# Kernel optimization log

Hardware: AMD Instinct MI355X
Metric: run time of the kernel (lower is better)

Reference implementation:

```python
import jax, jax.numpy as jnp
import numpy as np

D_BRICK = 512  # args.brick_vector_dimension
H = 512        # hidden width


def setup_inputs() -> dict:
    key = jax.random.key(0)
    ks = jax.random.split(key, 20)
    B, N = 4, 192

    def w(k, shape, fan_in):
        return jax.random.uniform(k, shape, jnp.float32, -1.0, 1.0) / np.sqrt(fan_in)

    return {
        "brick_vectors": jax.random.normal(ks[0], (B, N, D_BRICK), jnp.float32),
        "xy": jax.random.uniform(ks[1], (B, N, 2), jnp.float32),
        # linear_xy: 2 -> 512
        "W_xy": w(ks[2], (H, 2), 2), "b_xy": w(ks[3], (H,), 2),
        # linear_a: D -> 512
        "W_a": w(ks[4], (H, D_BRICK), D_BRICK), "b_a": w(ks[5], (H,), D_BRICK),
        # linear_b: 512 -> 512
        "W_b": w(ks[6], (H, H), H), "b_b": w(ks[7], (H,), H),
        # combination_a: 1024 -> 512
        "W_ca": w(ks[8], (H, 2 * H), 2 * H), "b_ca": w(ks[9], (H,), 2 * H),
        # combination_b: 512 -> 512
        "W_cb": w(ks[10], (H, H), H), "b_cb": w(ks[11], (H,), H),
        # combination_c: 512 -> 512
        "W_cc": w(ks[12], (H, H), H), "b_cc": w(ks[13], (H,), H),
        # edge_out: 512 -> 2
        "W_out": w(ks[14], (2, H), H), "b_out": w(ks[15], (2,), H),
    }


def reference(brick_vectors, xy, W_xy, b_xy, W_a, b_a, W_b, b_b,
              W_ca, b_ca, W_cb, b_cb, W_cc, b_cc, W_out, b_out):
    # per-brick feature MLP: (B, N, 512)
    f = jnp.einsum('bnd,hd->bnh', brick_vectors, W_a) + b_a \
        + jnp.einsum('bnt,ht->bnh', xy, W_xy) + b_xy
    f = jax.nn.relu(f)
    f = jax.nn.relu(jnp.einsum('bnh,gh->bng', f, W_b) + b_b)

    # combination_a on concat(f[b,j], f[b,i]) without materializing the
    # (B, N, N, 1024) tensor: split the weight into the two 512 halves.
    # edge[b,i,j] = cat(features_a, features_b) where features_a = f[b,j]
    # (expanded over dim 1) and features_b = f[b,i] (expanded over dim 2).
    W1, W2 = W_ca[:, :H], W_ca[:, H:]
    u = jnp.einsum('bnh,gh->bng', f, W1)  # contribution from f[b, j]
    v = jnp.einsum('bnh,gh->bng', f, W2)  # contribution from f[b, i]
    e = jax.nn.relu(u[:, None, :, :] + v[:, :, None, :] + b_ca)  # (B,N,N,512)

    e = jax.nn.relu(jnp.einsum('bijh,gh->bijg', e, W_cb) + b_cb)
    e = jax.nn.relu(jnp.einsum('bijh,gh->bijg', e, W_cc) + b_cc)
    return jnp.einsum('bijh,oh->bijo', e, W_out) + b_out  # (B, N, N, 2)
```

## Files before the change

### kernel.cpp

```cpp
#include <hip/hip_runtime.h>


typedef short  short8  __attribute__((ext_vector_type(8)));
typedef short  short4v __attribute__((ext_vector_type(4)));
typedef float  f32x4   __attribute__((ext_vector_type(4)));

#define LDSW 520

__device__ inline unsigned short f2bf(float x) {
  unsigned u = __float_as_uint(x);
  unsigned r = (u + 0x7FFFu + ((u >> 16) & 1u)) >> 16;
  return (unsigned short)r;
}

__device__ __host__ inline int wtile_off(int c, int k) {
  return ((c >> 4) * 16 + (k >> 5)) * 512 + (c & 15) * 32 + (k & 31);
}

template <int MT, int NT>
__device__ inline void zero_acc(f32x4 (&acc)[MT][NT]) {
#pragma unroll
  for (int mt = 0; mt < MT; ++mt)
#pragma unroll
    for (int nt = 0; nt < NT; ++nt) {
      f32x4 z = {0.f, 0.f, 0.f, 0.f};
      acc[mt][nt] = z;
    }
}

template <int MT, int NT>
__device__ inline void gemm_kloop(const short* E, const short* __restrict__ W,
                                  int lane, int nbase, f32x4 (&acc)[MT][NT]) {
  const int mrow = lane & 15, kg = lane >> 4;
  const short* El = E + mrow * LDSW + kg * 8;
  const short* Wl = W + (nbase >> 4) * 8192 + mrow * 32 + kg * 8;
  short8 wF[2][NT];
#pragma unroll
  for (int nt = 0; nt < NT; ++nt) wF[0][nt] = *(const short8*)(Wl + nt * 8192);
#pragma unroll
  for (int ks = 0; ks < 16; ++ks) {
    const int cur = ks & 1, nxt = cur ^ 1;
    if (ks < 15) {
      const int k1 = (ks + 1) * 512;
#pragma unroll
      for (int nt = 0; nt < NT; ++nt)
        wF[nxt][nt] = *(const short8*)(Wl + nt * 8192 + k1);
    }
    const int k0 = ks * 32;
    short8 e0 = *(const short8*)(El + k0);
#pragma unroll
    for (int mt = 0; mt < MT; ++mt) {
      const short8 ecur = e0;
      if (mt < MT - 1) e0 = *(const short8*)(El + (mt + 1) * 16 * LDSW + k0);
#pragma unroll
      for (int nt = 0; nt < NT; ++nt)
        acc[mt][nt] = __builtin_amdgcn_mfma_f32_16x16x32_bf16(
            wF[cur][nt], ecur, acc[mt][nt], 0, 0, 0);
    }
  }
}

template <int MT, int NT>
__device__ inline void store_relu_lds(short* E, const float* __restrict__ bias,
                                      int lane, int nbase, f32x4 (&acc)[MT][NT]) {
  const int mrow = lane & 15, kg = lane >> 4;
#pragma unroll
  for (int nt = 0; nt < NT; ++nt) {
    const int oc = nbase + nt * 16 + kg * 4;
    const float4 bs = *(const float4*)(bias + oc);
#pragma unroll
    for (int mt = 0; mt < MT; ++mt) {
      short4v s;
      s.x = (short)f2bf(fmaxf(acc[mt][nt][0] + bs.x, 0.f));
      s.y = (short)f2bf(fmaxf(acc[mt][nt][1] + bs.y, 0.f));
      s.z = (short)f2bf(fmaxf(acc[mt][nt][2] + bs.z, 0.f));
      s.w = (short)f2bf(fmaxf(acc[mt][nt][3] + bs.w, 0.f));
      *(short4v*)&E[(mt * 16 + mrow) * LDSW + oc] = s;
    }
  }
}

__global__ void prep_kernel(const float* __restrict__ Wa, const float* __restrict__ Wb,
                            const float* __restrict__ Wca, const float* __restrict__ Wcb,
                            const float* __restrict__ Wcc, const float* __restrict__ Wout,
                            short* __restrict__ outS) {
  const int tid = blockIdx.x * blockDim.x + threadIdx.x;
  const int stride = gridDim.x * blockDim.x;
  const int M = 262144;
  for (int i = tid; i < 6 * M + 1024; i += stride) {
    float x;
    int dst;
    if (i < M) {
      const int c = i >> 9, k = i & 511;
      x = Wa[i];
      dst = wtile_off(c, k);
    } else if (i < 2 * M) {
      const int t = i - M, c = t >> 9, k = t & 511;
      x = Wb[t];
      dst = M + wtile_off(c, k);
    } else if (i < 3 * M) {
      const int t = i - 2 * M, c = t >> 9, k = t & 511;
      x = Wca[c * 1024 + k];
      dst = 2 * M + wtile_off(c, k);
    } else if (i < 4 * M) {
      const int t = i - 3 * M, c = t >> 9, k = t & 511;
      x = Wca[c * 1024 + 512 + k];
      dst = 2 * M + wtile_off(512 + c, k);
    } else if (i < 5 * M) {
      const int t = i - 4 * M, c = t >> 9, k = t & 511;
      x = Wcb[t];
      dst = 4 * M + wtile_off(c, k);
    } else if (i < 6 * M) {
      const int t = i - 5 * M, c = t >> 9, k = t & 511;
      x = Wcc[t];
      dst = 5 * M + wtile_off(c, k);
    } else {
      x = Wout[i - 6 * M];
      dst = i;
    }
    outS[dst] = (short)f2bf(x);
  }
}

template <int MODE>
__global__ __launch_bounds__(256, 4) void node_layer(
    const void* __restrict__ Xin, const short* __restrict__ W,
    const float* __restrict__ bias, const float* __restrict__ xy,
    const float* __restrict__ Wxy, const float* __restrict__ bxy,
    void* __restrict__ Yout, float* __restrict__ vout, int colTiles) {
  __shared__ short X[64 * LDSW];
  __shared__ float xyl[128];
  const int tid = threadIdx.x, lane = tid & 63, wave = tid >> 6;
  const int rt = blockIdx.x / colTiles, ct = blockIdx.x % colTiles;
  const int row0 = rt * 64, c0 = ct * 64;

  if (MODE == 1) {
    const float* bv = (const float*)Xin;
    const int hc = (tid & 127) * 4, m0 = tid >> 7;
    for (int m = m0; m < 64; m += 2) {
      const float4 t = *(const float4*)(bv + (row0 + m) * 512 + hc);
      short4v s;
      s.x = (short)f2bf(t.x); s.y = (short)f2bf(t.y);
      s.z = (short)f2bf(t.z); s.w = (short)f2bf(t.w);
      *(short4v*)&X[m * LDSW + hc] = s;
    }
    if (tid < 128) xyl[tid] = xy[row0 * 2 + tid];
  } else {
    const short* xb = (const short*)Xin;
    const int hc = (tid & 63) * 8, m0 = tid >> 6;
    for (int m = m0; m < 64; m += 4)
      *(short8*)&X[m * LDSW + hc] = *(const short8*)(xb + (row0 + m) * 512 + hc);
  }
  __syncthreads();

  const int nbase = c0 + wave * 16;
  f32x4 acc[4][1];
  zero_acc<4, 1>(acc);
  gemm_kloop<4, 1>(X, W, lane, nbase, acc);

  const int mrow = lane & 15, kg = lane >> 4;
  const int oc = nbase + kg * 4;
  if (MODE == 3) {
    float* u = (float*)Yout;
#pragma unroll
    for (int mt = 0; mt < 4; ++mt) {
      const int row = row0 + mt * 16 + mrow;
      if (oc < 512) *(f32x4*)&u[row * 512 + oc] = acc[mt][0];
      else          *(f32x4*)&vout[row * 512 + oc - 512] = acc[mt][0];
    }
  } else {
    short* Y = (short*)Yout;
    const float4 bs = *(const float4*)(bias + oc);
    float b2[4] = {0.f, 0.f, 0.f, 0.f}, w0[4], w1[4];
    if (MODE == 1) {
      const float4 t = *(const float4*)(bxy + oc);
      b2[0] = t.x; b2[1] = t.y; b2[2] = t.z; b2[3] = t.w;
#pragma unroll
      for (int r = 0; r < 4; ++r) { w0[r] = Wxy[(oc + r) * 2]; w1[r] = Wxy[(oc + r) * 2 + 1]; }
    }
#pragma unroll
    for (int mt = 0; mt < 4; ++mt) {
      const int row = mt * 16 + mrow;
      short4v s;
#pragma unroll
      for (int r = 0; r < 4; ++r) {
        float xv = acc[mt][0][r] + ((const float*)&bs)[r];
        if (MODE == 1) xv += b2[r] + xyl[row * 2] * w0[r] + xyl[row * 2 + 1] * w1[r];
        ((short*)&s)[r] = (short)f2bf(fmaxf(xv, 0.f));
      }
      *(short4v*)&Y[(row0 + row) * 512 + oc] = s;
    }
  }
}

__global__ __launch_bounds__(512, 2) void edge_kernel(
    const float* __restrict__ u, const float* __restrict__ v,
    const short* __restrict__ Wcb, const short* __restrict__ Wcc,
    const short* __restrict__ Wout,
    const float* __restrict__ bca, const float* __restrict__ bcb,
    const float* __restrict__ bcc, const float* __restrict__ bout,
    float* __restrict__ out) {
  __shared__ short A[144 * LDSW];
  __shared__ float red[144 * 2 * 8];
  const int tid = threadIdx.x, lane = tid & 63, wave = tid >> 6;
  const int blk = blockIdx.x;
  const int b = blk >> 8, rem = blk & 255, ip = rem >> 2, jt = rem & 3;
  const float* urow0 = u + (b * 192 + jt * 48) * 512;
  const float* vrow0 = v + (b * 192 + ip * 3) * 512;

  {
    const int hc = (tid & 127) * 4, m0 = tid >> 7;
    const float4 v0 = *(const float4*)(vrow0 + hc);
    const float4 v1 = *(const float4*)(vrow0 + 512 + hc);
    const float4 v2 = *(const float4*)(vrow0 + 1024 + hc);
    const float4 bb = *(const float4*)(bca + hc);
#pragma unroll 4
    for (int m = m0; m < 144; m += 4) {
      const int ii = (m >= 96) ? 2 : (m >= 48 ? 1 : 0);
      const int jj = m - ii * 48;
      const float4 vv = (ii == 0) ? v0 : (ii == 1) ? v1 : v2;
      const float4 uu = *(const float4*)(urow0 + jj * 512 + hc);
      short4v s;
      s.x = (short)f2bf(fmaxf(uu.x + vv.x + bb.x, 0.f));
      s.y = (short)f2bf(fmaxf(uu.y + vv.y + bb.y, 0.f));
      s.z = (short)f2bf(fmaxf(uu.z + vv.z + bb.z, 0.f));
      s.w = (short)f2bf(fmaxf(uu.w + vv.w + bb.w, 0.f));
      *(short4v*)&A[m * LDSW + hc] = s;
    }
  }
  __syncthreads();

  const int nbase = wave * 64;
  f32x4 acc[9][4];

  zero_acc<9, 4>(acc);
  gemm_kloop<9, 4>(A, Wcb, lane, nbase, acc);
  __syncthreads();
  store_relu_lds<9, 4>(A, bcb, lane, nbase, acc);
  __syncthreads();

  zero_acc<9, 4>(acc);
  gemm_kloop<9, 4>(A, Wcc, lane, nbase, acc);
  __syncthreads();
  store_relu_lds<9, 4>(A, bcc, lane, nbase, acc);
  __syncthreads();

  f32x4 oacc[9];
#pragma unroll
  for (int mt = 0; mt < 9; ++mt) { f32x4 z = {0.f, 0.f, 0.f, 0.f}; oacc[mt] = z; }
  const int n = lane & 15, kg2 = lane >> 4;
#pragma unroll
  for (int kk = 0; kk < 2; ++kk) {
    const int k0 = wave * 64 + kk * 32 + kg2 * 8;
    short8 bf = {0, 0, 0, 0, 0, 0, 0, 0};
    if (n < 2) bf = *(const short8*)(Wout + n * 512 + k0);
#pragma unroll
    for (int mt = 0; mt < 9; ++mt) {
      const short8 af = *(const short8*)(A + (mt * 16 + n) * LDSW + k0);
      oacc[mt] = __builtin_amdgcn_mfma_f32_16x16x32_bf16(af, bf, oacc[mt], 0, 0, 0);
    }
  }
  if (n < 2) {
#pragma unroll
    for (int mt = 0; mt < 9; ++mt)
#pragma unroll
      for (int r = 0; r < 4; ++r) {
        const int row = mt * 16 + kg2 * 4 + r;
        red[(row * 2 + n) * 8 + wave] = oacc[mt][r];
      }
  }
  __syncthreads();
  if (tid < 288) {
    const int row = tid >> 1, o = tid & 1;
    float s = bout[o];
#pragma unroll
    for (int w = 0; w < 8; ++w) s += red[(row * 2 + o) * 8 + w];
    const int ii = (row >= 96) ? 2 : (row >= 48 ? 1 : 0);
    const int jj = row - ii * 48;
    out[((b * 192 + ip * 3 + ii) * 192 + jt * 48 + jj) * 2 + o] = s;
  }
}

extern "C" void kernel_launch(void* const* d_in, const int* in_sizes, int n_in,
                              void* d_out, int out_size, void* d_ws, size_t ws_size,
                              hipStream_t stream) {
  const float* bv   = (const float*)d_in[0];
  const float* xy   = (const float*)d_in[1];
  const float* Wxy  = (const float*)d_in[2];
  const float* bxy  = (const float*)d_in[3];
  const float* Wa   = (const float*)d_in[4];
  const float* ba   = (const float*)d_in[5];
  const float* Wb   = (const float*)d_in[6];
  const float* bb   = (const float*)d_in[7];
  const float* Wca  = (const float*)d_in[8];
  const float* bca  = (const float*)d_in[9];
  const float* Wcb  = (const float*)d_in[10];
  const float* bcb  = (const float*)d_in[11];
  const float* Wcc  = (const float*)d_in[12];
  const float* bcc  = (const float*)d_in[13];
  const float* Wout = (const float*)d_in[14];
  const float* bout = (const float*)d_in[15];
  float* out = (float*)d_out;

  short* S = (short*)d_ws;
  char* base = (char*)d_ws;
  short* WaB   = S;
  short* WbB   = S + 262144;
  short* WuvB  = S + 524288;
  short* WcbB  = S + 1048576;
  short* WccB  = S + 1310720;
  short* WoutB = S + 1572864;
  short* f1 = (short*)(base + 3147776);
  float* u  = (float*)(base + 3147776);
  short* f2 = (short*)(base + 4720640);
  float* v  = (float*)(base + 5507072);

  prep_kernel<<<512, 256, 0, stream>>>(Wa, Wb, Wca, Wcb, Wcc, Wout, S);
  node_layer<1><<<96, 256, 0, stream>>>(bv, WaB, ba, xy, Wxy, bxy, f1, nullptr, 8);
  node_layer<2><<<96, 256, 0, stream>>>(f1, WbB, bb, nullptr, nullptr, nullptr, f2, nullptr, 8);
  node_layer<3><<<192, 256, 0, stream>>>(f2, WuvB, nullptr, nullptr, nullptr, nullptr, u, v, 16);
  edge_kernel<<<1024, 512, 0, stream>>>(u, v, WcbB, WccB, WoutB, bca, bcb, bcc, bout, out);
}
```

Baseline: 262.2 us.

## Fuse three node MLP layers into one kernel keeping activations in LDS

Replaces the three node_layer launches with a single node_fused kernel. Each block of 512 threads owns 32 rows and runs all three GEMMs back to back, passing intermediate activations through two shared-memory buffers instead of global memory. This removes two kernel launches and the global round trips for f1 and f2. In exchange only 24 blocks run, so most of the GPU's compute units sit idle during this phase.

```diff
diff --git a/kernel.cpp b/kernel.cpp
--- a/kernel.cpp
+++ b/kernel.cpp
@@ -122,73 +122,84 @@
   }
 }
 
-template <int MODE>
-__global__ __launch_bounds__(256, 4) void node_layer(
-    const void* __restrict__ Xin, const short* __restrict__ W,
-    const float* __restrict__ bias, const float* __restrict__ xy,
-    const float* __restrict__ Wxy, const float* __restrict__ bxy,
-    void* __restrict__ Yout, float* __restrict__ vout, int colTiles) {
-  __shared__ short X[64 * LDSW];
-  __shared__ float xyl[128];
+__global__ __launch_bounds__(512, 2) void node_fused(
+    const float* __restrict__ bv, const short* __restrict__ WaB,
+    const short* __restrict__ WbB, const short* __restrict__ WuvB,
+    const float* __restrict__ ba, const float* __restrict__ bb,
+    const float* __restrict__ xy, const float* __restrict__ Wxy,
+    const float* __restrict__ bxy, float* __restrict__ u, float* __restrict__ v) {
+  __shared__ short X[2][32 * LDSW];
+  __shared__ float xyl[64];
   const int tid = threadIdx.x, lane = tid & 63, wave = tid >> 6;
-  const int rt = blockIdx.x / colTiles, ct = blockIdx.x % colTiles;
-  const int row0 = rt * 64, c0 = ct * 64;
-
-  if (MODE == 1) {
-    const float* bv = (const float*)Xin;
+  const int row0 = blockIdx.x * 32;
+  const int mrow = lane & 15, kg = lane >> 4;
+
+  {
     const int hc = (tid & 127) * 4, m0 = tid >> 7;
-    for (int m = m0; m < 64; m += 2) {
+#pragma unroll
+    for (int m = m0; m < 32; m += 4) {
       const float4 t = *(const float4*)(bv + (row0 + m) * 512 + hc);
       short4v s;
       s.x = (short)f2bf(t.x); s.y = (short)f2bf(t.y);
       s.z = (short)f2bf(t.z); s.w = (short)f2bf(t.w);
-      *(short4v*)&X[m * LDSW + hc] = s;
-    }
-    if (tid < 128) xyl[tid] = xy[row0 * 2 + tid];
-  } else {
-    const short* xb = (const short*)Xin;
-    const int hc = (tid & 63) * 8, m0 = tid >> 6;
-    for (int m = m0; m < 64; m += 4)
-      *(short8*)&X[m * LDSW + hc] = *(const short8*)(xb + (row0 + m) * 512 + hc);
-  }
-  __syncthreads();
-
-  const int nbase = c0 + wave * 16;
-  f32x4 acc[4][1];
-  zero_acc<4, 1>(acc);
-  gemm_kloop<4, 1>(X, W, lane, nbase, acc);
-
-  const int mrow = lane & 15, kg = lane >> 4;
-  const int oc = nbase + kg * 4;
-  if (MODE == 3) {
-    float* u = (float*)Yout;
-#pragma unroll
-    for (int mt = 0; mt < 4; ++mt) {
-      const int row = row0 + mt * 16 + mrow;
-      if (oc < 512) *(f32x4*)&u[row * 512 + oc] = acc[mt][0];
-      else          *(f32x4*)&vout[row * 512 + oc - 512] = acc[mt][0];
-    }
-  } else {
-    short* Y = (short*)Yout;
-    const float4 bs = *(const float4*)(bias + oc);
-    float b2[4] = {0.f, 0.f, 0.f, 0.f}, w0[4], w1[4];
-    if (MODE == 1) {
-      const float4 t = *(const float4*)(bxy + oc);
-      b2[0] = t.x; b2[1] = t.y; b2[2] = t.z; b2[3] = t.w;
-#pragma unroll
-      for (int r = 0; r < 4; ++r) { w0[r] = Wxy[(oc + r) * 2]; w1[r] = Wxy[(oc + r) * 2 + 1]; }
-    }
-#pragma unroll
-    for (int mt = 0; mt < 4; ++mt) {
-      const int row = mt * 16 + mrow;
-      short4v s;
+      *(short4v*)&X[0][m * LDSW + hc] = s;
+    }
+    if (tid < 64) xyl[tid] = xy[row0 * 2 + tid];
+  }
+  __syncthreads();
+
+  {
+    f32x4 acc[2][4];
+    zero_acc<2, 4>(acc);
+    gemm_kloop<2, 4>(X[0], WaB, lane, wave * 64, acc);
+#pragma unroll
+    for (int nt = 0; nt < 4; ++nt) {
+      const int oc = wave * 64 + nt * 16 + kg * 4;
+      const float4 bs = *(const float4*)(ba + oc);
+      const float4 bx = *(const float4*)(bxy + oc);
+      float w0[4], w1[4];
 #pragma unroll
       for (int r = 0; r < 4; ++r) {
-        float xv = acc[mt][0][r] + ((const float*)&bs)[r];
-        if (MODE == 1) xv += b2[r] + xyl[row * 2] * w0[r] + xyl[row * 2 + 1] * w1[r];
-        ((short*)&s)[r] = (short)f2bf(fmaxf(xv, 0.f));
+        w0[r] = Wxy[(oc + r) * 2];
+        w1[r] = Wxy[(oc + r) * 2 + 1];
       }
-      *(short4v*)&Y[(row0 + row) * 512 + oc] = s;
+#pragma unroll
+      for (int mt = 0; mt < 2; ++mt) {
+        const int row = mt * 16 + mrow;
+        short4v s;
+#pragma unroll
+        for (int r = 0; r < 4; ++r) {
+          float xv = acc[mt][nt][r] + ((const float*)&bs)[r] + ((const float*)&bx)[r]
+                   + xyl[row * 2] * w0[r] + xyl[row * 2 + 1] * w1[r];
+          ((short*)&s)[r] = (short)f2bf(fmaxf(xv, 0.f));
+        }
+        *(short4v*)&X[1][row * LDSW + oc] = s;
+      }
+    }
+  }
+  __syncthreads();
+
+  {
+    f32x4 acc[2][4];
+    zero_acc<2, 4>(acc);
+    gemm_kloop<2, 4>(X[1], WbB, lane, wave * 64, acc);
+    store_relu_lds<2, 4>(X[0], bb, lane, wave * 64, acc);
+  }
+  __syncthreads();
+
+  {
+    f32x4 acc[2][8];
+    zero_acc<2, 8>(acc);
+    gemm_kloop<2, 8>(X[0], WuvB, lane, wave * 128, acc);
+#pragma unroll
+    for (int nt = 0; nt < 8; ++nt) {
+      const int oc = wave * 128 + nt * 16 + kg * 4;
+#pragma unroll
+      for (int mt = 0; mt < 2; ++mt) {
+        const int row = row0 + mt * 16 + mrow;
+        if (oc < 512) *(f32x4*)&u[row * 512 + oc] = acc[mt][nt];
+        else          *(f32x4*)&v[row * 512 + oc - 512] = acc[mt][nt];
+      }
     }
   }
 }
@@ -310,14 +321,10 @@
   short* WcbB  = S + 1048576;
   short* WccB  = S + 1310720;
   short* WoutB = S + 1572864;
-  short* f1 = (short*)(base + 3147776);
   float* u  = (float*)(base + 3147776);
-  short* f2 = (short*)(base + 4720640);
   float* v  = (float*)(base + 5507072);
 
   prep_kernel<<<512, 256, 0, stream>>>(Wa, Wb, Wca, Wcb, Wcc, Wout, S);
-  node_layer<1><<<96, 256, 0, stream>>>(bv, WaB, ba, xy, Wxy, bxy, f1, nullptr, 8);
-  node_layer<2><<<96, 256, 0, stream>>>(f1, WbB, bb, nullptr, nullptr, nullptr, f2, nullptr, 8);
-  node_layer<3><<<192, 256, 0, stream>>>(f2, WuvB, nullptr, nullptr, nullptr, nullptr, u, v, 16);
+  node_fused<<<24, 512, 0, stream>>>(bv, WaB, WbB, WuvB, ba, bb, xy, Wxy, bxy, u, v);
   edge_kernel<<<1024, 512, 0, stream>>>(u, v, WcbB, WccB, WoutB, bca, bcb, bcc, bout, out);
 }
```

Result: no change. 267.2 us (+1.9%).

## Fold weight prep into node layers and read fp32 weights directly

Applied to the files above, without the earlier changes.

Removes the separate prep kernel. The node-layer GEMMs now load fp32 weights directly and convert them to bf16 in registers, and the edge-kernel weight conversion moves into the first node_layer launch. It also uses the packed v_cvt_pk_bf16_f32 instruction for ReLU+pack, deepens the weight prefetch in the edge GEMM to a triple buffer, and folds the bias into the v rows before the edge fill loop. The aim is to drop one launch and its full-weight conversion pass. In exchange the node layers read twice the weight bytes, and the first layer does extra conversion work; the triple buffer also adds register pressure in the edge kernel.

```diff
diff --git a/kernel.cpp b/kernel.cpp
--- a/kernel.cpp
+++ b/kernel.cpp
@@ -11,6 +11,18 @@
   unsigned u = __float_as_uint(x);
   unsigned r = (u + 0x7FFFu + ((u >> 16) & 1u)) >> 16;
   return (unsigned short)r;
+}
+
+__device__ inline unsigned cvt_pk_bf16(float lo, float hi) {
+  unsigned d;
+  asm("v_cvt_pk_bf16_f32 %0, %1, %2" : "=v"(d) : "v"(lo), "v"(hi));
+  return d;
+}
+__device__ inline uint2 relu_pack4(float x0, float x1, float x2, float x3) {
+  uint2 s;
+  s.x = cvt_pk_bf16(fmaxf(x0, 0.f), fmaxf(x1, 0.f));
+  s.y = cvt_pk_bf16(fmaxf(x2, 0.f), fmaxf(x3, 0.f));
+  return s;
 }
 
 __device__ __host__ inline int wtile_off(int c, int k) {
@@ -34,28 +46,64 @@
   const int mrow = lane & 15, kg = lane >> 4;
   const short* El = E + mrow * LDSW + kg * 8;
   const short* Wl = W + (nbase >> 4) * 8192 + mrow * 32 + kg * 8;
-  short8 wF[2][NT];
-#pragma unroll
-  for (int nt = 0; nt < NT; ++nt) wF[0][nt] = *(const short8*)(Wl + nt * 8192);
+  short8 wF[3][NT];
+#pragma unroll
+  for (int nt = 0; nt < NT; ++nt) {
+    wF[0][nt] = *(const short8*)(Wl + nt * 8192);
+    wF[1][nt] = *(const short8*)(Wl + nt * 8192 + 512);
+  }
+#pragma unroll
+  for (int ks = 0; ks < 16; ++ks) {
+    const int cur = ks % 3;
+    if (ks < 14) {
+      const int nx2 = (ks + 2) % 3, k2 = (ks + 2) * 512;
+#pragma unroll
+      for (int nt = 0; nt < NT; ++nt)
+        wF[nx2][nt] = *(const short8*)(Wl + nt * 8192 + k2);
+    }
+    const int k0 = ks * 32;
+    short8 e0 = *(const short8*)(El + k0);
+#pragma unroll
+    for (int mt = 0; mt < MT; ++mt) {
+      const short8 ecur = e0;
+      if (mt < MT - 1) e0 = *(const short8*)(El + (mt + 1) * 16 * LDSW + k0);
+#pragma unroll
+      for (int nt = 0; nt < NT; ++nt)
+        acc[mt][nt] = __builtin_amdgcn_mfma_f32_16x16x32_bf16(
+            wF[cur][nt], ecur, acc[mt][nt], 0, 0, 0);
+    }
+  }
+}
+
+template <int MT, int WSTRIDE>
+__device__ inline void gemm_kloop_wf32(const short* E, const float* __restrict__ W,
+                                       int lane, int colbase, f32x4 (&acc)[MT][1]) {
+  const int mrow = lane & 15, kg = lane >> 4;
+  const short* El = E + mrow * LDSW + kg * 8;
+  const float* Wl = W + (colbase + mrow) * WSTRIDE + kg * 8;
+  f32x4 wA[2][2];
+  wA[0][0] = *(const f32x4*)(Wl);
+  wA[0][1] = *(const f32x4*)(Wl + 4);
 #pragma unroll
   for (int ks = 0; ks < 16; ++ks) {
     const int cur = ks & 1, nxt = cur ^ 1;
     if (ks < 15) {
-      const int k1 = (ks + 1) * 512;
-#pragma unroll
-      for (int nt = 0; nt < NT; ++nt)
-        wF[nxt][nt] = *(const short8*)(Wl + nt * 8192 + k1);
-    }
+      wA[nxt][0] = *(const f32x4*)(Wl + (ks + 1) * 32);
+      wA[nxt][1] = *(const f32x4*)(Wl + (ks + 1) * 32 + 4);
+    }
+    short8 wf;
+    unsigned* wfu = (unsigned*)&wf;
+    wfu[0] = cvt_pk_bf16(wA[cur][0][0], wA[cur][0][1]);
+    wfu[1] = cvt_pk_bf16(wA[cur][0][2], wA[cur][0][3]);
+    wfu[2] = cvt_pk_bf16(wA[cur][1][0], wA[cur][1][1]);
+    wfu[3] = cvt_pk_bf16(wA[cur][1][2], wA[cur][1][3]);
     const int k0 = ks * 32;
     short8 e0 = *(const short8*)(El + k0);
 #pragma unroll
     for (int mt = 0; mt < MT; ++mt) {
       const short8 ecur = e0;
       if (mt < MT - 1) e0 = *(const short8*)(El + (mt + 1) * 16 * LDSW + k0);
-#pragma unroll
-      for (int nt = 0; nt < NT; ++nt)
-        acc[mt][nt] = __builtin_amdgcn_mfma_f32_16x16x32_bf16(
-            wF[cur][nt], ecur, acc[mt][nt], 0, 0, 0);
+      acc[mt][0] = __builtin_amdgcn_mfma_f32_16x16x32_bf16(wf, ecur, acc[mt][0], 0, 0, 0);
     }
   }
 }
@@ -70,79 +118,56 @@
     const float4 bs = *(const float4*)(bias + oc);
 #pragma unroll
     for (int mt = 0; mt < MT; ++mt) {
-      short4v s;
-      s.x = (short)f2bf(fmaxf(acc[mt][nt][0] + bs.x, 0.f));
-      s.y = (short)f2bf(fmaxf(acc[mt][nt][1] + bs.y, 0.f));
-      s.z = (short)f2bf(fmaxf(acc[mt][nt][2] + bs.z, 0.f));
-      s.w = (short)f2bf(fmaxf(acc[mt][nt][3] + bs.w, 0.f));
-      *(short4v*)&E[(mt * 16 + mrow) * LDSW + oc] = s;
-    }
-  }
-}
-
-__global__ void prep_kernel(const float* __restrict__ Wa, const float* __restrict__ Wb,
-                            const float* __restrict__ Wca, const float* __restrict__ Wcb,
-                            const float* __restrict__ Wcc, const float* __restrict__ Wout,
-                            short* __restrict__ outS) {
-  const int tid = blockIdx.x * blockDim.x + threadIdx.x;
-  const int stride = gridDim.x * blockDim.x;
-  const int M = 262144;
-  for (int i = tid; i < 6 * M + 1024; i += stride) {
-    float x;
-    int dst;
-    if (i < M) {
-      const int c = i >> 9, k = i & 511;
-      x = Wa[i];
-      dst = wtile_off(c, k);
-    } else if (i < 2 * M) {
-      const int t = i - M, c = t >> 9, k = t & 511;
-      x = Wb[t];
-      dst = M + wtile_off(c, k);
-    } else if (i < 3 * M) {
-      const int t = i - 2 * M, c = t >> 9, k = t & 511;
-      x = Wca[c * 1024 + k];
-      dst = 2 * M + wtile_off(c, k);
-    } else if (i < 4 * M) {
-      const int t = i - 3 * M, c = t >> 9, k = t & 511;
-      x = Wca[c * 1024 + 512 + k];
-      dst = 2 * M + wtile_off(512 + c, k);
-    } else if (i < 5 * M) {
-      const int t = i - 4 * M, c = t >> 9, k = t & 511;
-      x = Wcb[t];
-      dst = 4 * M + wtile_off(c, k);
-    } else if (i < 6 * M) {
-      const int t = i - 5 * M, c = t >> 9, k = t & 511;
-      x = Wcc[t];
-      dst = 5 * M + wtile_off(c, k);
-    } else {
-      x = Wout[i - 6 * M];
-      dst = i;
-    }
-    outS[dst] = (short)f2bf(x);
+      uint2 s = relu_pack4(acc[mt][nt][0] + bs.x, acc[mt][nt][1] + bs.y,
+                           acc[mt][nt][2] + bs.z, acc[mt][nt][3] + bs.w);
+      *(uint2*)&E[(mt * 16 + mrow) * LDSW + oc] = s;
+    }
   }
 }
 
 template <int MODE>
 __global__ __launch_bounds__(256, 4) void node_layer(
-    const void* __restrict__ Xin, const short* __restrict__ W,
+    const void* __restrict__ Xin, const float* __restrict__ W,
     const float* __restrict__ bias, const float* __restrict__ xy,
     const float* __restrict__ Wxy, const float* __restrict__ bxy,
-    void* __restrict__ Yout, float* __restrict__ vout, int colTiles) {
+    void* __restrict__ Yout, float* __restrict__ vout, int colTiles,
+    const float* __restrict__ Wcb, const float* __restrict__ Wcc,
+    const float* __restrict__ Wout, short* __restrict__ edgeW) {
   __shared__ short X[64 * LDSW];
   __shared__ float xyl[128];
   const int tid = threadIdx.x, lane = tid & 63, wave = tid >> 6;
   const int rt = blockIdx.x / colTiles, ct = blockIdx.x % colTiles;
   const int row0 = rt * 64, c0 = ct * 64;
+  const int mrow = lane & 15, kg = lane >> 4;
+
+  if (MODE == 1) {
+    const int M = 262144;
+    const int gtid = blockIdx.x * blockDim.x + tid;
+    const int gstride = gridDim.x * blockDim.x;
+    for (int i = gtid; i < 2 * M + 1024; i += gstride) {
+      float x; int dst;
+      if (i < M) {
+        const int c = i >> 9, k = i & 511;
+        x = Wcb[i]; dst = wtile_off(c, k);
+      } else if (i < 2 * M) {
+        const int t = i - M, c = t >> 9, k = t & 511;
+        x = Wcc[t]; dst = M + wtile_off(c, k);
+      } else {
+        x = Wout[i - 2 * M]; dst = i;
+      }
+      edgeW[dst] = (short)f2bf(x);
+    }
+  }
 
   if (MODE == 1) {
     const float* bv = (const float*)Xin;
     const int hc = (tid & 127) * 4, m0 = tid >> 7;
     for (int m = m0; m < 64; m += 2) {
       const float4 t = *(const float4*)(bv + (row0 + m) * 512 + hc);
-      short4v s;
-      s.x = (short)f2bf(t.x); s.y = (short)f2bf(t.y);
-      s.z = (short)f2bf(t.z); s.w = (short)f2bf(t.w);
-      *(short4v*)&X[m * LDSW + hc] = s;
+      uint2 s;
+      s.x = cvt_pk_bf16(t.x, t.y);
+      s.y = cvt_pk_bf16(t.z, t.w);
+      *(uint2*)&X[m * LDSW + hc] = s;
     }
     if (tid < 128) xyl[tid] = xy[row0 * 2 + tid];
   } else {
@@ -156,9 +181,15 @@
   const int nbase = c0 + wave * 16;
   f32x4 acc[4][1];
   zero_acc<4, 1>(acc);
-  gemm_kloop<4, 1>(X, W, lane, nbase, acc);
-
-  const int mrow = lane & 15, kg = lane >> 4;
+
+  if (MODE == 3) {
+    const float* Wbase = (c0 < 512) ? W : (W + 512);
+    const int colbase = (c0 < 512) ? nbase : (nbase - 512);
+    gemm_kloop_wf32<4, 1024>(X, Wbase, lane, colbase, acc);
+  } else {
+    gemm_kloop_wf32<4, 512>(X, W, lane, nbase, acc);
+  }
+
   const int oc = nbase + kg * 4;
   if (MODE == 3) {
     float* u = (float*)Yout;
@@ -181,14 +212,14 @@
 #pragma unroll
     for (int mt = 0; mt < 4; ++mt) {
       const int row = mt * 16 + mrow;
-      short4v s;
+      float xv[4];
 #pragma unroll
       for (int r = 0; r < 4; ++r) {
-        float xv = acc[mt][0][r] + ((const float*)&bs)[r];
-        if (MODE == 1) xv += b2[r] + xyl[row * 2] * w0[r] + xyl[row * 2 + 1] * w1[r];
-        ((short*)&s)[r] = (short)f2bf(fmaxf(xv, 0.f));
+        xv[r] = acc[mt][0][r] + ((const float*)&bs)[r];
+        if (MODE == 1) xv[r] += b2[r] + xyl[row * 2] * w0[r] + xyl[row * 2 + 1] * w1[r];
       }
-      *(short4v*)&Y[(row0 + row) * 512 + oc] = s;
+      uint2 s = relu_pack4(xv[0], xv[1], xv[2], xv[3]);
+      *(uint2*)&Y[(row0 + row) * 512 + oc] = s;
     }
   }
 }
@@ -210,22 +241,22 @@
 
   {
     const int hc = (tid & 127) * 4, m0 = tid >> 7;
-    const float4 v0 = *(const float4*)(vrow0 + hc);
-    const float4 v1 = *(const float4*)(vrow0 + 512 + hc);
-    const float4 v2 = *(const float4*)(vrow0 + 1024 + hc);
     const float4 bb = *(const float4*)(bca + hc);
+    const float4 a0 = *(const float4*)(vrow0 + hc);
+    const float4 a1 = *(const float4*)(vrow0 + 512 + hc);
+    const float4 a2 = *(const float4*)(vrow0 + 1024 + hc);
+    float4 vb0, vb1, vb2;
+    vb0.x = a0.x + bb.x; vb0.y = a0.y + bb.y; vb0.z = a0.z + bb.z; vb0.w = a0.w + bb.w;
+    vb1.x = a1.x + bb.x; vb1.y = a1.y + bb.y; vb1.z = a1.z + bb.z; vb1.w = a1.w + bb.w;
+    vb2.x = a2.x + bb.x; vb2.y = a2.y + bb.y; vb2.z = a2.z + bb.z; vb2.w = a2.w + bb.w;
 #pragma unroll 4
     for (int m = m0; m < 144; m += 4) {
       const int ii = (m >= 96) ? 2 : (m >= 48 ? 1 : 0);
       const int jj = m - ii * 48;
-      const float4 vv = (ii == 0) ? v0 : (ii == 1) ? v1 : v2;
+      const float4 vv = (ii == 0) ? vb0 : (ii == 1) ? vb1 : vb2;
       const float4 uu = *(const float4*)(urow0 + jj * 512 + hc);
-      short4v s;
-      s.x = (short)f2bf(fmaxf(uu.x + vv.x + bb.x, 0.f));
-      s.y = (short)f2bf(fmaxf(uu.y + vv.y + bb.y, 0.f));
-      s.z = (short)f2bf(fmaxf(uu.z + vv.z + bb.z, 0.f));
-      s.w = (short)f2bf(fmaxf(uu.w + vv.w + bb.w, 0.f));
-      *(short4v*)&A[m * LDSW + hc] = s;
+      uint2 s = relu_pack4(uu.x + vv.x, uu.y + vv.y, uu.z + vv.z, uu.w + vv.w);
+      *(uint2*)&A[m * LDSW + hc] = s;
     }
   }
   __syncthreads();
@@ -304,20 +335,19 @@
 
   short* S = (short*)d_ws;
   char* base = (char*)d_ws;
-  short* WaB   = S;
-  short* WbB   = S + 262144;
-  short* WuvB  = S + 524288;
-  short* WcbB  = S + 1048576;
-  short* WccB  = S + 1310720;
-  short* WoutB = S + 1572864;
-  short* f1 = (short*)(base + 3147776);
-  float* u  = (float*)(base + 3147776);
-  short* f2 = (short*)(base + 4720640);
-  float* v  = (float*)(base + 5507072);
-
-  prep_kernel<<<512, 256, 0, stream>>>(Wa, Wb, Wca, Wcb, Wcc, Wout, S);
-  node_layer<1><<<96, 256, 0, stream>>>(bv, WaB, ba, xy, Wxy, bxy, f1, nullptr, 8);
-  node_layer<2><<<96, 256, 0, stream>>>(f1, WbB, bb, nullptr, nullptr, nullptr, f2, nullptr, 8);
-  node_layer<3><<<192, 256, 0, stream>>>(f2, WuvB, nullptr, nullptr, nullptr, nullptr, u, v, 16);
+  short* WcbB  = S;
+  short* WccB  = S + 262144;
+  short* WoutB = S + 524288;
+  short* f2 = (short*)(base + 1050624);
+  short* f1 = (short*)(base + 1837056);
+  float* u  = (float*)(base + 1837056);
+  float* v  = (float*)(base + 3409920);
+
+  node_layer<1><<<96, 256, 0, stream>>>(bv, Wa, ba, xy, Wxy, bxy, f1, nullptr, 8,
+                                        Wcb, Wcc, Wout, S);
+  node_layer<2><<<96, 256, 0, stream>>>(f1, Wb, bb, nullptr, nullptr, nullptr, f2,
+                                        nullptr, 8, nullptr, nullptr, nullptr, nullptr);
+  node_layer<3><<<192, 256, 0, stream>>>(f2, Wca, nullptr, nullptr, nullptr, nullptr,
+                                         u, v, 16, nullptr, nullptr, nullptr, nullptr);
   edge_kernel<<<1024, 512, 0, stream>>>(u, v, WcbB, WccB, WoutB, bca, bcb, bcc, bout, out);
 }
```

Result: slower. 274.9 us (+4.8%).

## Shrink edge tiles to 64 rows and use packed bf16 convert instruction

Applied to the files above, without the earlier changes.

The edge kernel now processes 64 edge rows per block (one i, 64 j's) instead of 144, with a 2304-block grid and launch bounds raised to 4 blocks per CU. The smaller LDS footprint and accumulator count are meant to raise occupancy and shrink the register file per wave. The trade is that each block amortizes its weight reads from global/L2 over fewer rows. Separately, manual round-to-nearest bf16 conversion is replaced with the hardware v_cvt_pk_bf16_f32 instruction to cut ALU work in epilogues.

```diff
diff --git a/kernel.cpp b/kernel.cpp
--- a/kernel.cpp
+++ b/kernel.cpp
@@ -11,6 +11,18 @@
   unsigned u = __float_as_uint(x);
   unsigned r = (u + 0x7FFFu + ((u >> 16) & 1u)) >> 16;
   return (unsigned short)r;
+}
+
+__device__ inline unsigned cvt_pk_bf16(float lo, float hi) {
+  unsigned d;
+  asm("v_cvt_pk_bf16_f32 %0, %1, %2" : "=v"(d) : "v"(lo), "v"(hi));
+  return d;
+}
+__device__ inline uint2 relu_pack4(float x0, float x1, float x2, float x3) {
+  uint2 s;
+  s.x = cvt_pk_bf16(fmaxf(x0, 0.f), fmaxf(x1, 0.f));
+  s.y = cvt_pk_bf16(fmaxf(x2, 0.f), fmaxf(x3, 0.f));
+  return s;
 }
 
 __device__ __host__ inline int wtile_off(int c, int k) {
@@ -70,12 +82,9 @@
     const float4 bs = *(const float4*)(bias + oc);
 #pragma unroll
     for (int mt = 0; mt < MT; ++mt) {
-      short4v s;
-      s.x = (short)f2bf(fmaxf(acc[mt][nt][0] + bs.x, 0.f));
-      s.y = (short)f2bf(fmaxf(acc[mt][nt][1] + bs.y, 0.f));
-      s.z = (short)f2bf(fmaxf(acc[mt][nt][2] + bs.z, 0.f));
-      s.w = (short)f2bf(fmaxf(acc[mt][nt][3] + bs.w, 0.f));
-      *(short4v*)&E[(mt * 16 + mrow) * LDSW + oc] = s;
+      uint2 s = relu_pack4(acc[mt][nt][0] + bs.x, acc[mt][nt][1] + bs.y,
+                           acc[mt][nt][2] + bs.z, acc[mt][nt][3] + bs.w);
+      *(uint2*)&E[(mt * 16 + mrow) * LDSW + oc] = s;
     }
   }
 }
@@ -139,10 +148,10 @@
     const int hc = (tid & 127) * 4, m0 = tid >> 7;
     for (int m = m0; m < 64; m += 2) {
       const float4 t = *(const float4*)(bv + (row0 + m) * 512 + hc);
-      short4v s;
-      s.x = (short)f2bf(t.x); s.y = (short)f2bf(t.y);
-      s.z = (short)f2bf(t.z); s.w = (short)f2bf(t.w);
-      *(short4v*)&X[m * LDSW + hc] = s;
+      uint2 s;
+      s.x = cvt_pk_bf16(t.x, t.y);
+      s.y = cvt_pk_bf16(t.z, t.w);
+      *(uint2*)&X[m * LDSW + hc] = s;
     }
     if (tid < 128) xyl[tid] = xy[row0 * 2 + tid];
   } else {
@@ -181,73 +190,66 @@
 #pragma unroll
     for (int mt = 0; mt < 4; ++mt) {
       const int row = mt * 16 + mrow;
-      short4v s;
+      float xv[4];
 #pragma unroll
       for (int r = 0; r < 4; ++r) {
-        float xv = acc[mt][0][r] + ((const float*)&bs)[r];
-        if (MODE == 1) xv += b2[r] + xyl[row * 2] * w0[r] + xyl[row * 2 + 1] * w1[r];
-        ((short*)&s)[r] = (short)f2bf(fmaxf(xv, 0.f));
+        xv[r] = acc[mt][0][r] + ((const float*)&bs)[r];
+        if (MODE == 1) xv[r] += b2[r] + xyl[row * 2] * w0[r] + xyl[row * 2 + 1] * w1[r];
       }
-      *(short4v*)&Y[(row0 + row) * 512 + oc] = s;
-    }
-  }
-}
-
-__global__ __launch_bounds__(512, 2) void edge_kernel(
+      uint2 s = relu_pack4(xv[0], xv[1], xv[2], xv[3]);
+      *(uint2*)&Y[(row0 + row) * 512 + oc] = s;
+    }
+  }
+}
+
+__global__ __launch_bounds__(512, 4) void edge_kernel(
     const float* __restrict__ u, const float* __restrict__ v,
     const short* __restrict__ Wcb, const short* __restrict__ Wcc,
     const short* __restrict__ Wout,
     const float* __restrict__ bca, const float* __restrict__ bcb,
     const float* __restrict__ bcc, const float* __restrict__ bout,
     float* __restrict__ out) {
-  __shared__ short A[144 * LDSW];
-  __shared__ float red[144 * 2 * 8];
+  __shared__ short A[64 * LDSW];
+  __shared__ float red[64 * 2 * 8];
   const int tid = threadIdx.x, lane = tid & 63, wave = tid >> 6;
   const int blk = blockIdx.x;
-  const int b = blk >> 8, rem = blk & 255, ip = rem >> 2, jt = rem & 3;
-  const float* urow0 = u + (b * 192 + jt * 48) * 512;
-  const float* vrow0 = v + (b * 192 + ip * 3) * 512;
+  const int b = blk / 576, rem = blk % 576, i = rem / 3, jt = rem % 3;
+  const float* urow0 = u + (b * 192 + jt * 64) * 512;
+  const float* vrow  = v + (b * 192 + i) * 512;
 
   {
     const int hc = (tid & 127) * 4, m0 = tid >> 7;
-    const float4 v0 = *(const float4*)(vrow0 + hc);
-    const float4 v1 = *(const float4*)(vrow0 + 512 + hc);
-    const float4 v2 = *(const float4*)(vrow0 + 1024 + hc);
     const float4 bb = *(const float4*)(bca + hc);
+    const float4 a0 = *(const float4*)(vrow + hc);
+    float4 vb;
+    vb.x = a0.x + bb.x; vb.y = a0.y + bb.y; vb.z = a0.z + bb.z; vb.w = a0.w + bb.w;
 #pragma unroll 4
-    for (int m = m0; m < 144; m += 4) {
-      const int ii = (m >= 96) ? 2 : (m >= 48 ? 1 : 0);
-      const int jj = m - ii * 48;
-      const float4 vv = (ii == 0) ? v0 : (ii == 1) ? v1 : v2;
-      const float4 uu = *(const float4*)(urow0 + jj * 512 + hc);
-      short4v s;
-      s.x = (short)f2bf(fmaxf(uu.x + vv.x + bb.x, 0.f));
-      s.y = (short)f2bf(fmaxf(uu.y + vv.y + bb.y, 0.f));
-      s.z = (short)f2bf(fmaxf(uu.z + vv.z + bb.z, 0.f));
-      s.w = (short)f2bf(fmaxf(uu.w + vv.w + bb.w, 0.f));
-      *(short4v*)&A[m * LDSW + hc] = s;
+    for (int m = m0; m < 64; m += 4) {
+      const float4 uu = *(const float4*)(urow0 + m * 512 + hc);
+      uint2 s = relu_pack4(uu.x + vb.x, uu.y + vb.y, uu.z + vb.z, uu.w + vb.w);
+      *(uint2*)&A[m * LDSW + hc] = s;
     }
   }
   __syncthreads();
 
   const int nbase = wave * 64;
-  f32x4 acc[9][4];
-
-  zero_acc<9, 4>(acc);
-  gemm_kloop<9, 4>(A, Wcb, lane, nbase, acc);
-  __syncthreads();
-  store_relu_lds<9, 4>(A, bcb, lane, nbase, acc);
-  __syncthreads();
-
-  zero_acc<9, 4>(acc);
-  gemm_kloop<9, 4>(A, Wcc, lane, nbase, acc);
-  __syncthreads();
-  store_relu_lds<9, 4>(A, bcc, lane, nbase, acc);
-  __syncthreads();
-
-  f32x4 oacc[9];
-#pragma unroll
-  for (int mt = 0; mt < 9; ++mt) { f32x4 z = {0.f, 0.f, 0.f, 0.f}; oacc[mt] = z; }
+  f32x4 acc[4][4];
+
+  zero_acc<4, 4>(acc);
+  gemm_kloop<4, 4>(A, Wcb, lane, nbase, acc);
+  __syncthreads();
+  store_relu_lds<4, 4>(A, bcb, lane, nbase, acc);
+  __syncthreads();
+
+  zero_acc<4, 4>(acc);
+  gemm_kloop<4, 4>(A, Wcc, lane, nbase, acc);
+  __syncthreads();
+  store_relu_lds<4, 4>(A, bcc, lane, nbase, acc);
+  __syncthreads();
+
+  f32x4 oacc[4];
+#pragma unroll
+  for (int mt = 0; mt < 4; ++mt) { f32x4 z = {0.f, 0.f, 0.f, 0.f}; oacc[mt] = z; }
   const int n = lane & 15, kg2 = lane >> 4;
 #pragma unroll
   for (int kk = 0; kk < 2; ++kk) {
@@ -255,14 +257,14 @@
     short8 bf = {0, 0, 0, 0, 0, 0, 0, 0};
     if (n < 2) bf = *(const short8*)(Wout + n * 512 + k0);
 #pragma unroll
-    for (int mt = 0; mt < 9; ++mt) {
+    for (int mt = 0; mt < 4; ++mt) {
       const short8 af = *(const short8*)(A + (mt * 16 + n) * LDSW + k0);
       oacc[mt] = __builtin_amdgcn_mfma_f32_16x16x32_bf16(af, bf, oacc[mt], 0, 0, 0);
     }
   }
   if (n < 2) {
 #pragma unroll
-    for (int mt = 0; mt < 9; ++mt)
+    for (int mt = 0; mt < 4; ++mt)
 #pragma unroll
       for (int r = 0; r < 4; ++r) {
         const int row = mt * 16 + kg2 * 4 + r;
@@ -270,14 +272,12 @@
       }
   }
   __syncthreads();
-  if (tid < 288) {
+  if (tid < 128) {
     const int row = tid >> 1, o = tid & 1;
     float s = bout[o];
 #pragma unroll
     for (int w = 0; w < 8; ++w) s += red[(row * 2 + o) * 8 + w];
-    const int ii = (row >= 96) ? 2 : (row >= 48 ? 1 : 0);
-    const int jj = row - ii * 48;
-    out[((b * 192 + ip * 3 + ii) * 192 + jt * 48 + jj) * 2 + o] = s;
+    out[((b * 192 + i) * 192 + jt * 64 + row) * 2 + o] = s;
   }
 }
 
@@ -319,5 +319,5 @@
   node_layer<1><<<96, 256, 0, stream>>>(bv, WaB, ba, xy, Wxy, bxy, f1, nullptr, 8);
   node_layer<2><<<96, 256, 0, stream>>>(f1, WbB, bb, nullptr, nullptr, nullptr, f2, nullptr, 8);
   node_layer<3><<<192, 256, 0, stream>>>(f2, WuvB, nullptr, nullptr, nullptr, nullptr, u, v, 16);
-  edge_kernel<<<1024, 512, 0, stream>>>(u, v, WcbB, WccB, WoutB, bca, bcb, bcc, bout, out);
-}
+  edge_kernel<<<2304, 512, 0, stream>>>(u, v, WcbB, WccB, WoutB, bca, bcb, bcc, bout, out);
+}
```

New measurement: 324.3 us. 1.24x slower.
